# Optimization experiments

Measured on AMD Instinct MI355X. Metric: run time of the kernel, lower is better.

## Reference

```python
import jax, jax.numpy as jnp
import numpy as np

BN_EPS = 1e-5
HIDDEN = 64
NUM_LAYERS = 8


def setup_inputs() -> dict:
    key = jax.random.key(0)
    ks = jax.random.split(key, 24)
    N, E, G = 100000, 1600000, 500
    H, L = HIDDEN, NUM_LAYERS
    rn = lambda k, s, sc=0.1: jax.random.normal(k, s, jnp.float32) * sc
    un = lambda k, s: jax.random.uniform(k, s, jnp.float32, 0.5, 1.5)
    inp = {}
    inp["x"] = jax.random.normal(ks[0], (N, 1), jnp.float32)
    inp["edge_index"] = jax.random.randint(ks[1], (2, E), 0, N, jnp.int32)
    inp["batch"] = jnp.sort(jax.random.randint(ks[2], (N,), 0, G, jnp.int32))
    inp["num_graphs"] = G
    inp["eps"] = rn(ks[3], (L,))
    inp["W1_first"] = rn(ks[4], (1, H))
    inp["W1_rest"] = rn(ks[5], (L - 1, H, H))
    inp["b1"] = rn(ks[6], (L, H))
    inp["g1"] = un(ks[7], (L, H))
    inp["be1"] = rn(ks[8], (L, H))
    inp["m1"] = rn(ks[9], (L, H))
    inp["v1"] = un(ks[10], (L, H))
    inp["W2"] = rn(ks[11], (L, H, H))
    inp["b2"] = rn(ks[12], (L, H))
    inp["g2"] = un(ks[13], (L, H))
    inp["be2"] = rn(ks[14], (L, H))
    inp["m2"] = rn(ks[15], (L, H))
    inp["v2"] = un(ks[16], (L, H))
    inp["lin1_w"] = rn(ks[17], (L * H, H), 0.05)
    inp["lin1_b"] = rn(ks[18], (H,))
    inp["lin2_w"] = rn(ks[19], (H, 3))
    inp["lin2_b"] = rn(ks[20], (3,))
    return inp


def _bn(h, g, b, m, v):
    # BatchNorm1d in eval mode: affine normalize with running stats
    return (h - m) * jax.lax.rsqrt(v + BN_EPS) * g + b


def reference(x, edge_index, batch, num_graphs, eps, W1_first, W1_rest, b1, g1,
              be1, m1, v1, W2, b2, g2, be2, m2, v2, lin1_w, lin1_b, lin2_w, lin2_b):
    src, dst = edge_index[0], edge_index[1]
    N = x.shape[0]
    h = x
    xs = []
    for i in range(NUM_LAYERS):
        # GINConv: scatter-add neighbor aggregation + (1+eps)*self, then MLP
        agg = jax.ops.segment_sum(h[src], dst, num_segments=N)  # [N, H_in]
        z = (1.0 + eps[i]) * h + agg
        W1 = W1_first if i == 0 else W1_rest[i - 1]
        z = jnp.maximum(z @ W1 + b1[i], 0.0)
        z = _bn(z, g1[i], be1[i], m1[i], v1[i])
        z = jnp.maximum(z @ W2[i] + b2[i], 0.0)
        z = _bn(z, g2[i], be2[i], m2[i], v2[i])
        h = z
        xs.append(h)
    jk = jnp.concatenate(xs, axis=-1)  # [N, L*H] JumpingKnowledge 'cat'
    sums = jax.ops.segment_sum(jk, batch, num_segments=num_graphs)
    counts = jax.ops.segment_sum(jnp.ones((N,), jk.dtype), batch, num_segments=num_graphs)
    pooled = sums / jnp.maximum(counts, 1.0)[:, None]  # global_mean_pool
    h = jnp.maximum(pooled @ lin1_w + lin1_b, 0.0)
    # dropout is identity in eval mode
    logits = h @ lin2_w + lin2_b
    return jax.nn.log_softmax(logits, axis=-1)
```

## Files before the change

kernel.cpp:

```cpp
#include <hip/hip_runtime.h>
#include <hip/hip_bf16.h>
#include <math.h>


typedef unsigned int uint;
typedef unsigned short ushort;
typedef __attribute__((ext_vector_type(8))) short short8;
typedef __attribute__((ext_vector_type(4))) float floatx4;
typedef __attribute__((ext_vector_type(4))) uint uintx4;

#define BBITS 10
#define BCAP 20480
#define BMASK ((1 << BBITS) - 1)

__device__ __forceinline__ float bf_lo(uint w) { return __uint_as_float(w << 16); }
__device__ __forceinline__ float bf_hi(uint w) { return __uint_as_float(w & 0xffff0000u); }

__device__ __forceinline__ ushort f2bf(float x) {
  __hip_bfloat16 h = __float2bfloat16(x);
  return *(ushort*)&h;
}
__device__ __forceinline__ float bf2f(ushort u) { return __uint_as_float((uint)u << 16); }

__device__ __forceinline__ uint pack_bf16(float a, float b) {
  return (uint)f2bf(a) | ((uint)f2bf(b) << 16);
}

__device__ __forceinline__ void split8(float4 u0, float4 u1, short8& hi, short8& lo) {
  float v0 = u0.x, v1 = u0.y, v2 = u0.z, v3 = u0.w;
  float v4 = u1.x, v5 = u1.y, v6 = u1.z, v7 = u1.w;
  ushort h0 = f2bf(v0), h1 = f2bf(v1), h2 = f2bf(v2), h3 = f2bf(v3);
  ushort h4 = f2bf(v4), h5 = f2bf(v5), h6 = f2bf(v6), h7 = f2bf(v7);
  hi[0] = (short)h0; hi[1] = (short)h1; hi[2] = (short)h2; hi[3] = (short)h3;
  hi[4] = (short)h4; hi[5] = (short)h5; hi[6] = (short)h6; hi[7] = (short)h7;
  lo[0] = (short)f2bf(v0 - bf2f(h0)); lo[1] = (short)f2bf(v1 - bf2f(h1));
  lo[2] = (short)f2bf(v2 - bf2f(h2)); lo[3] = (short)f2bf(v3 - bf2f(h3));
  lo[4] = (short)f2bf(v4 - bf2f(h4)); lo[5] = (short)f2bf(v5 - bf2f(h5));
  lo[6] = (short)f2bf(v6 - bf2f(h6)); lo[7] = (short)f2bf(v7 - bf2f(h7));
}


__global__ void init_bc_kernel(int* __restrict__ bc, int NB) {
  int b = threadIdx.x;
  if (b < NB) bc[b * 16] = b * BCAP;
}

__global__ __launch_bounds__(1024) void bin_edges_kernel(
    const int* __restrict__ src, const int* __restrict__ dst, int* __restrict__ bc,
    uint* __restrict__ arena, int E) {
  __shared__ int cnt[128], base[128];
  for (long chunk = (long)blockIdx.x * 4096; chunk < E; chunk += (long)gridDim.x * 4096) {
    if (threadIdx.x < 128) cnt[threadIdx.x] = 0;
    __syncthreads();
    uint v[4];
    int b[4], r[4];
#pragma unroll
    for (int u = 0; u < 4; ++u) {
      long e = chunk + threadIdx.x + u * 1024;
      if (e < E) {
        int s = src[e];
        int d = dst[e];
        b[u] = d >> BBITS;
        v[u] = ((uint)s << BBITS) | (uint)(d & BMASK);
        r[u] = atomicAdd(&cnt[b[u]], 1);
      }
    }
    __syncthreads();
    if (threadIdx.x < 128)
      base[threadIdx.x] = cnt[threadIdx.x] ? atomicAdd(&bc[threadIdx.x * 16], cnt[threadIdx.x]) : 0;
    __syncthreads();
#pragma unroll
    for (int u = 0; u < 4; ++u) {
      long e = chunk + threadIdx.x + u * 1024;
      if (e < E) arena[base[b[u]] + r[u]] = v[u];
    }
    __syncthreads();
  }
}

__global__ __launch_bounds__(1024) void bucket_count_kernel(
    const uint* __restrict__ arena, const int* __restrict__ bc,
    int* __restrict__ deg, int N) {
  __shared__ int hist[1 << BBITS];
  int b = blockIdx.x;
  int lo = b << BBITS;
  int hi = min(lo + (1 << BBITS), N);
  hist[threadIdx.x] = 0;
  __syncthreads();
  int cnt = bc[b * 16] - b * BCAP;
  const uint* ad = arena + (size_t)b * BCAP;
  for (int i = threadIdx.x; i < cnt; i += 1024) atomicAdd(&hist[ad[i] & BMASK], 1);
  __syncthreads();
  if (lo + (int)threadIdx.x < hi) deg[lo + threadIdx.x] = hist[threadIdx.x];
}

__global__ __launch_bounds__(1024) void bucket_scatter_kernel(
    const uint* __restrict__ arena, const int* __restrict__ bc,
    const int* __restrict__ rp, int* __restrict__ col, int N) {
  __shared__ int cur[1 << BBITS];
  int b = blockIdx.x;
  int lo = b << BBITS;
  int hi = min(lo + (1 << BBITS), N);
  if (lo + (int)threadIdx.x < hi) cur[threadIdx.x] = rp[lo + threadIdx.x];
  __syncthreads();
  int cnt = bc[b * 16] - b * BCAP;
  const uint* ad = arena + (size_t)b * BCAP;
  for (int i = threadIdx.x; i < cnt; i += 1024) {
    uint v = ad[i];
    int pos = atomicAdd(&cur[v & BMASK], 1);
    col[pos] = (int)(v >> BBITS);
  }
}

__global__ void scan_blocksums(const int* __restrict__ deg, int* __restrict__ bsum, int N) {
  __shared__ int red[256];
  int i = blockIdx.x * 256 + threadIdx.x;
  red[threadIdx.x] = (i < N) ? deg[i] : 0;
  __syncthreads();
  for (int off = 128; off > 0; off >>= 1) {
    if (threadIdx.x < off) red[threadIdx.x] += red[threadIdx.x + off];
    __syncthreads();
  }
  if (threadIdx.x == 0) bsum[blockIdx.x] = red[0];
}

__global__ void scan_bsum(const int* __restrict__ bsum, int* __restrict__ boff,
                          int* __restrict__ rp_last, int B) {
  __shared__ int tmp[1024];
  int t = threadIdx.x;
  int v = (t < B) ? bsum[t] : 0;
  tmp[t] = v;
  __syncthreads();
  for (int off = 1; off < 1024; off <<= 1) {
    int u = (t >= off) ? tmp[t - off] : 0;
    __syncthreads();
    tmp[t] += u;
    __syncthreads();
  }
  if (t < B) boff[t] = tmp[t] - v;
  if (t == 1023) *rp_last = tmp[1023];
}

__global__ void scan_final(const int* __restrict__ deg, const int* __restrict__ boff,
                           int* __restrict__ rp, int N) {
  __shared__ int tmp[256];
  int i = blockIdx.x * 256 + threadIdx.x;
  int v = (i < N) ? deg[i] : 0;
  tmp[threadIdx.x] = v;
  __syncthreads();
  for (int off = 1; off < 256; off <<= 1) {
    int u = (threadIdx.x >= off) ? tmp[threadIdx.x - off] : 0;
    __syncthreads();
    tmp[threadIdx.x] += u;
    __syncthreads();
  }
  if (i < N) rp[i] = boff[blockIdx.x] + tmp[threadIdx.x] - v;
}

__global__ void graph_bounds_kernel(const int* __restrict__ batch, int* __restrict__ gs,
                                    int N, int G) {
  int n = blockIdx.x * 256 + threadIdx.x;
  if (n >= N) return;
  int b = batch[n];
  int bp = (n == 0) ? -1 : batch[n - 1];
  for (int g = bp + 1; g <= b; ++g) gs[g] = n;
  if (n == N - 1)
    for (int g = b + 1; g <= G; ++g) gs[g] = N;
}

__global__ void prepack_w_kernel(const float* __restrict__ W1_rest,
                                 const float* __restrict__ W2, ushort* __restrict__ wp) {
  int l = blockIdx.x >> 1, g = blockIdx.x & 1;
  const float* W;
  if (g == 0) {
    if (l == 0) return;
    W = W1_rest + (size_t)(l - 1) * 4096;
  } else {
    W = W2 + (size_t)l * 4096;
  }
  ushort* out = wp + (size_t)(l * 2 + g) * 8192;
  for (int idx = threadIdx.x; idx < 4096; idx += blockDim.x) {
    int j = idx & 7, lane = (idx >> 3) & 63, ks = (idx >> 9) & 1, nt = (idx >> 10) & 3;
    int k = ks * 32 + (lane >> 4) * 8 + j;
    int n = nt * 16 + (lane & 15);
    float w = W[k * 64 + n];
    ushort hi = f2bf(w);
    ushort lo = f2bf(w - bf2f(hi));
    size_t base = (size_t)((nt * 2 + ks) * 2) * 512 + lane * 8 + j;
    out[base] = hi;
    out[base + 512] = lo;
  }
}

__global__ __launch_bounds__(256, 8) void agg_kernel(
    const ushort* __restrict__ hb, const int* __restrict__ rp,
    const int* __restrict__ col, const float* __restrict__ eps,
    int layer, ushort* __restrict__ zb, int N) {
  int lane = threadIdx.x & 63;
  int g = lane >> 3;
  int r = lane & 7;
  int wave = blockIdx.x * (blockDim.x >> 6) + (threadIdx.x >> 6);
  int nwaves = gridDim.x * (blockDim.x >> 6);
  float ep = 1.0f + eps[layer];
  for (int n = wave * 2; n < N; n += nwaves * 2) {
    int n0 = __builtin_amdgcn_readfirstlane(n);
    int n1 = n0 + 1;
    int beg0 = rp[n0];
    int end0 = rp[n0 + 1];
    int end1 = (n1 < N) ? rp[n1 + 1] : end0;
    float a0[8] = {0.f, 0.f, 0.f, 0.f, 0.f, 0.f, 0.f, 0.f};
    float a1[8] = {0.f, 0.f, 0.f, 0.f, 0.f, 0.f, 0.f, 0.f};
    float b0[8] = {0.f, 0.f, 0.f, 0.f, 0.f, 0.f, 0.f, 0.f};
    float b1v[8] = {0.f, 0.f, 0.f, 0.f, 0.f, 0.f, 0.f, 0.f};
    int e0 = beg0 + g;
    int e1 = end0 + g;
    while (e0 < end0 || e1 < end1) {
      if (e0 < end0) {
        int s = col[e0];
        uint4 w = ((const uint4*)(hb + (long)s * 64))[r];
        a0[0] += bf_lo(w.x); a0[1] += bf_hi(w.x);
        a0[2] += bf_lo(w.y); a0[3] += bf_hi(w.y);
        a0[4] += bf_lo(w.z); a0[5] += bf_hi(w.z);
        a0[6] += bf_lo(w.w); a0[7] += bf_hi(w.w);
      }
      if (e0 + 8 < end0) {
        int s = col[e0 + 8];
        uint4 w = ((const uint4*)(hb + (long)s * 64))[r];
        a1[0] += bf_lo(w.x); a1[1] += bf_hi(w.x);
        a1[2] += bf_lo(w.y); a1[3] += bf_hi(w.y);
        a1[4] += bf_lo(w.z); a1[5] += bf_hi(w.z);
        a1[6] += bf_lo(w.w); a1[7] += bf_hi(w.w);
      }
      if (e1 < end1) {
        int s = col[e1];
        uint4 w = ((const uint4*)(hb + (long)s * 64))[r];
        b0[0] += bf_lo(w.x); b0[1] += bf_hi(w.x);
        b0[2] += bf_lo(w.y); b0[3] += bf_hi(w.y);
        b0[4] += bf_lo(w.z); b0[5] += bf_hi(w.z);
        b0[6] += bf_lo(w.w); b0[7] += bf_hi(w.w);
      }
      if (e1 + 8 < end1) {
        int s = col[e1 + 8];
        uint4 w = ((const uint4*)(hb + (long)s * 64))[r];
        b1v[0] += bf_lo(w.x); b1v[1] += bf_hi(w.x);
        b1v[2] += bf_lo(w.y); b1v[3] += bf_hi(w.y);
        b1v[4] += bf_lo(w.z); b1v[5] += bf_hi(w.z);
        b1v[6] += bf_lo(w.w); b1v[7] += bf_hi(w.w);
      }
      e0 += 16; e1 += 16;
    }
#pragma unroll
    for (int j = 0; j < 8; ++j) { a0[j] += a1[j]; b0[j] += b1v[j]; }
#pragma unroll
    for (int m = 8; m <= 32; m <<= 1) {
#pragma unroll
      for (int j = 0; j < 8; ++j) {
        a0[j] += __shfl_xor(a0[j], m, 64);
        b0[j] += __shfl_xor(b0[j], m, 64);
      }
    }
    if (g == 0) {
      uint4 hv = ((const uint4*)(hb + (long)n0 * 64))[r];
      float v0 = fmaf(ep, bf_lo(hv.x), a0[0]), v1 = fmaf(ep, bf_hi(hv.x), a0[1]);
      float v2 = fmaf(ep, bf_lo(hv.y), a0[2]), v3 = fmaf(ep, bf_hi(hv.y), a0[3]);
      float v4 = fmaf(ep, bf_lo(hv.z), a0[4]), v5 = fmaf(ep, bf_hi(hv.z), a0[5]);
      float v6 = fmaf(ep, bf_lo(hv.w), a0[6]), v7 = fmaf(ep, bf_hi(hv.w), a0[7]);
      uintx4 w;
      w.x = pack_bf16(v0, v1); w.y = pack_bf16(v2, v3);
      w.z = pack_bf16(v4, v5); w.w = pack_bf16(v6, v7);
      __builtin_nontemporal_store(w, (uintx4*)(zb + (size_t)n0 * 64 + r * 8));
    } else if (g == 1 && n1 < N) {
      uint4 hv = ((const uint4*)(hb + (long)n1 * 64))[r];
      float v0 = fmaf(ep, bf_lo(hv.x), b0[0]), v1 = fmaf(ep, bf_hi(hv.x), b0[1]);
      float v2 = fmaf(ep, bf_lo(hv.y), b0[2]), v3 = fmaf(ep, bf_hi(hv.y), b0[3]);
      float v4 = fmaf(ep, bf_lo(hv.z), b0[4]), v5 = fmaf(ep, bf_hi(hv.z), b0[5]);
      float v6 = fmaf(ep, bf_lo(hv.w), b0[6]), v7 = fmaf(ep, bf_hi(hv.w), b0[7]);
      uintx4 w;
      w.x = pack_bf16(v0, v1); w.y = pack_bf16(v2, v3);
      w.z = pack_bf16(v4, v5); w.w = pack_bf16(v6, v7);
      __builtin_nontemporal_store(w, (uintx4*)(zb + (size_t)n1 * 64 + r * 8));
    }
  }
}

__global__ __launch_bounds__(512) void mfma_mlp_kernel(
    const ushort* __restrict__ zb, const float* __restrict__ z0,
    const float* __restrict__ W1f, ushort* __restrict__ hout,
    const ushort* __restrict__ wp1, const ushort* __restrict__ wp2,
    const float* __restrict__ b1, const float* __restrict__ g1,
    const float* __restrict__ be1, const float* __restrict__ m1,
    const float* __restrict__ v1,
    const float* __restrict__ b2, const float* __restrict__ g2,
    const float* __restrict__ be2, const float* __restrict__ m2,
    const float* __restrict__ v2,
    const int* __restrict__ batch, float* __restrict__ pooled,
    int layer, int skip1, int N) {
  __shared__ float bnp[6][64];
  __shared__ float w1fl[64];
  __shared__ float sbuf[128][68];
  __shared__ int batchl[128];
  int tid = threadIdx.x;
  int blockbase = blockIdx.x * 128;
  if (tid < 64) {
    bnp[0][tid] = b1[tid];
    float s1 = g1[tid] * rsqrtf(v1[tid] + 1e-5f);
    bnp[1][tid] = s1;
    bnp[2][tid] = be1[tid] - m1[tid] * s1;
    bnp[3][tid] = b2[tid];
    float s2 = g2[tid] * rsqrtf(v2[tid] + 1e-5f);
    bnp[4][tid] = s2;
    bnp[5][tid] = be2[tid] - m2[tid] * s2;
    if (skip1) w1fl[tid] = W1f[tid];
  }
  if (tid < 128) batchl[tid] = (blockbase + tid < N) ? batch[blockbase + tid] : -1;
  __syncthreads();
  int wave = tid >> 6, lane = tid & 63;
  int q = lane >> 4, c = lane & 15;
  int base = blockbase + wave * 16;
  int srow = wave * 16;

  short8 ahi0, alo0, ahi1, alo1;
  if (!skip1) {
    {
      long row = base + c;
      if (row >= N) row = N - 1;
      const ushort* zr = zb + row * 64;
      ahi0 = __builtin_nontemporal_load((const short8*)(zr + q * 8));
      ahi1 = __builtin_nontemporal_load((const short8*)(zr + 32 + q * 8));
    }
    floatx4 acc[4];
#pragma unroll
    for (int nt = 0; nt < 4; ++nt) acc[nt] = (floatx4){0.f, 0.f, 0.f, 0.f};
#pragma unroll
    for (int nt = 0; nt < 4; ++nt) {
#pragma unroll
      for (int ks = 0; ks < 2; ++ks) {
        const ushort* fb = wp1 + ((nt * 2 + ks) * 2) * 512 + lane * 8;
        short8 bh = *(const short8*)fb;
        short8 bl = *(const short8*)(fb + 512);
        short8 ah = ks ? ahi1 : ahi0;
        acc[nt] = __builtin_amdgcn_mfma_f32_16x16x32_bf16(ah, bh, acc[nt], 0, 0, 0);
        acc[nt] = __builtin_amdgcn_mfma_f32_16x16x32_bf16(ah, bl, acc[nt], 0, 0, 0);
      }
    }
#pragma unroll
    for (int nt = 0; nt < 4; ++nt) {
      int feat = nt * 16 + c;
      float s1 = bnp[1][feat], o1 = bnp[2][feat], bb = bnp[0][feat];
#pragma unroll
      for (int r = 0; r < 4; ++r) {
        float y = fmaxf(acc[nt][r] + bb, 0.f);
        sbuf[srow + q * 4 + r][feat] = fmaf(y, s1, o1);
      }
    }
    float4 u0 = *(const float4*)&sbuf[srow + c][q * 8];
    float4 u1 = *(const float4*)&sbuf[srow + c][q * 8 + 4];
    split8(u0, u1, ahi0, alo0);
    u0 = *(const float4*)&sbuf[srow + c][32 + q * 8];
    u1 = *(const float4*)&sbuf[srow + c][32 + q * 8 + 4];
    split8(u0, u1, ahi1, alo1);
  } else {
    long row = base + c;
    if (row >= N) row = N - 1;
    float zv = z0[row];
    float4 t00, t01, t10, t11;
    {
      float tv[8];
#pragma unroll
      for (int j = 0; j < 8; ++j) {
        int k = q * 8 + j;
        float y = fmaxf(fmaf(zv, w1fl[k], bnp[0][k]), 0.f);
        tv[j] = fmaf(y, bnp[1][k], bnp[2][k]);
      }
      t00 = make_float4(tv[0], tv[1], tv[2], tv[3]);
      t01 = make_float4(tv[4], tv[5], tv[6], tv[7]);
#pragma unroll
      for (int j = 0; j < 8; ++j) {
        int k = 32 + q * 8 + j;
        float y = fmaxf(fmaf(zv, w1fl[k], bnp[0][k]), 0.f);
        tv[j] = fmaf(y, bnp[1][k], bnp[2][k]);
      }
      t10 = make_float4(tv[0], tv[1], tv[2], tv[3]);
      t11 = make_float4(tv[4], tv[5], tv[6], tv[7]);
    }
    split8(t00, t01, ahi0, alo0);
    split8(t10, t11, ahi1, alo1);
  }

  floatx4 acc2[4];
#pragma unroll
  for (int nt = 0; nt < 4; ++nt) acc2[nt] = (floatx4){0.f, 0.f, 0.f, 0.f};
#pragma unroll
  for (int nt = 0; nt < 4; ++nt) {
#pragma unroll
    for (int ks = 0; ks < 2; ++ks) {
      const ushort* fb = wp2 + ((nt * 2 + ks) * 2) * 512 + lane * 8;
      short8 bh = *(const short8*)fb;
      short8 bl = *(const short8*)(fb + 512);
      short8 ah = ks ? ahi1 : ahi0;
      short8 al = ks ? alo1 : alo0;
      acc2[nt] = __builtin_amdgcn_mfma_f32_16x16x32_bf16(ah, bh, acc2[nt], 0, 0, 0);
      acc2[nt] = __builtin_amdgcn_mfma_f32_16x16x32_bf16(al, bh, acc2[nt], 0, 0, 0);
      acc2[nt] = __builtin_amdgcn_mfma_f32_16x16x32_bf16(ah, bl, acc2[nt], 0, 0, 0);
    }
  }

#pragma unroll
  for (int nt = 0; nt < 4; ++nt) {
    int feat = nt * 16 + c;
    float s2 = bnp[4][feat], o2 = bnp[5][feat], bb = bnp[3][feat];
#pragma unroll
    for (int r = 0; r < 4; ++r) {
      int node = base + q * 4 + r;
      float val = 0.f;
      if (node < N) {
        float y = fmaxf(acc2[nt][r] + bb, 0.f);
        val = fmaf(y, s2, o2);
      }
      sbuf[srow + q * 4 + r][feat] = val;
    }
  }
  __syncthreads();

#pragma unroll
  for (int it = 0; it < 2; ++it) {
    int chunk = tid + it * 512;
    int row = chunk >> 3, c8 = chunk & 7;
    int node = blockbase + row;
    if (node < N) {
      const float* sp = &sbuf[row][c8 * 8];
      uintx4 w;
      w.x = pack_bf16(sp[0], sp[1]);
      w.y = pack_bf16(sp[2], sp[3]);
      w.z = pack_bf16(sp[4], sp[5]);
      w.w = pack_bf16(sp[6], sp[7]);
      *(uintx4*)(hout + (long)node * 64 + c8 * 8) = w;
    }
  }

  if (tid < 256) {
    int j = tid & 63;
    int quarter = tid >> 6;
    int nvalid = N - blockbase;
    if (nvalid > 128) nvalid = 128;
    int i = quarter * 32;
    int iend = i + 32;
    if (iend > nvalid) iend = nvalid;
    while (i < iend) {
      int g = batchl[i];
      float s = 0.f;
      while (i < iend && batchl[i] == g) { s += sbuf[i][j]; ++i; }
      atomicAdd(&pooled[(size_t)g * 512 + layer * 64 + j], s);
    }
  }
}

__global__ void z0_kernel(const float* __restrict__ x, const int* __restrict__ rp,
                          const int* __restrict__ col, const float* __restrict__ eps,
                          float* __restrict__ z0, int N) {
  int n = blockIdx.x * blockDim.x + threadIdx.x;
  if (n >= N) return;
  int beg = rp[n], end = rp[n + 1];
  float a = 0.f;
  for (int e = beg; e < end; ++e) a += x[col[e]];
  z0[n] = fmaf(1.0f + eps[0], x[n], a);
}

__global__ __launch_bounds__(64) void final_kernel(
    const float* __restrict__ pooled, const int* __restrict__ gs,
    const float* __restrict__ lin1_w, const float* __restrict__ lin1_b,
    const float* __restrict__ lin2_w, const float* __restrict__ lin2_b,
    float* __restrict__ out, int G) {
  int g = blockIdx.x;
  int j = threadIdx.x;
  float inv = 1.0f / fmaxf((float)(gs[g + 1] - gs[g]), 1.0f);
  __shared__ float p[512];
  for (int t = j; t < 512; t += 64) p[t] = pooled[(long)g * 512 + t] * inv;
  __syncthreads();
  float a0 = lin1_b[j], a1 = 0.f, a2 = 0.f, a3 = 0.f;
  for (int k = 0; k < 512; k += 4) {
    a0 = fmaf(p[k + 0], lin1_w[(k + 0) * 64 + j], a0);
    a1 = fmaf(p[k + 1], lin1_w[(k + 1) * 64 + j], a1);
    a2 = fmaf(p[k + 2], lin1_w[(k + 2) * 64 + j], a2);
    a3 = fmaf(p[k + 3], lin1_w[(k + 3) * 64 + j], a3);
  }
  float hv = fmaxf((a0 + a1) + (a2 + a3), 0.f);
  __shared__ float hb[64];
  hb[j] = hv;
  __syncthreads();
  __shared__ float lg[3];
  if (j < 3) {
    float a = lin2_b[j];
#pragma unroll
    for (int k = 0; k < 64; ++k) a = fmaf(hb[k], lin2_w[k * 3 + j], a);
    lg[j] = a;
  }
  __syncthreads();
  if (j < 3) {
    float mx = fmaxf(fmaxf(lg[0], lg[1]), lg[2]);
    float lse = mx + logf(expf(lg[0] - mx) + expf(lg[1] - mx) + expf(lg[2] - mx));
    out[g * 3 + j] = lg[j] - lse;
  }
}

extern "C" void kernel_launch(void* const* d_in, const int* in_sizes, int n_in,
                              void* d_out, int out_size, void* d_ws, size_t ws_size,
                              hipStream_t stream) {
  const float* x        = (const float*)d_in[0];
  const int*   edge     = (const int*)d_in[1];
  const int*   batch    = (const int*)d_in[2];
  const float* eps      = (const float*)d_in[4];
  const float* W1_first = (const float*)d_in[5];
  const float* W1_rest  = (const float*)d_in[6];
  const float* b1       = (const float*)d_in[7];
  const float* g1       = (const float*)d_in[8];
  const float* be1      = (const float*)d_in[9];
  const float* m1       = (const float*)d_in[10];
  const float* v1       = (const float*)d_in[11];
  const float* W2       = (const float*)d_in[12];
  const float* b2       = (const float*)d_in[13];
  const float* g2       = (const float*)d_in[14];
  const float* be2      = (const float*)d_in[15];
  const float* m2       = (const float*)d_in[16];
  const float* v2       = (const float*)d_in[17];
  const float* lin1_w   = (const float*)d_in[18];
  const float* lin1_b   = (const float*)d_in[19];
  const float* lin2_w   = (const float*)d_in[20];
  const float* lin2_b   = (const float*)d_in[21];

  int N = in_sizes[0];
  int E = in_sizes[1] / 2;
  int G = out_size / 3;
  const int* esrc = edge;
  const int* edst = edge + E;
  int NB = (N + (1 << BBITS) - 1) >> BBITS;
  if (NB > 128) NB = 128;

  size_t off = 0;
  auto alloc = [&](size_t bytes) -> char* {
    char* p = (char*)d_ws + off;
    off += (bytes + 255) & ~(size_t)255;
    return p;
  };
  int SB = (N + 255) / 256;
  int*    deg    = (int*)alloc((size_t)N * 4);
  int*    rp     = (int*)alloc((size_t)(N + 1) * 4);
  int*    col    = (int*)alloc((size_t)E * 4);
  int*    bsum   = (int*)alloc((size_t)SB * 4);
  int*    boff   = (int*)alloc((size_t)SB * 4);
  int*    bc     = (int*)alloc((size_t)128 * 16 * 4);
  uint*   arena  = (uint*)alloc((size_t)NB * BCAP * 4);
  int*    gs     = (int*)alloc((size_t)(G + 1) * 4);
  ushort* wpack  = (ushort*)alloc((size_t)16 * 8192 * 2);
  float*  z0buf  = (float*)alloc((size_t)N * 4);
  ushort* zbuf   = (ushort*)alloc((size_t)N * 64 * 2);
  ushort* hA     = (ushort*)alloc((size_t)N * 64 * 2);
  ushort* hB     = (ushort*)alloc((size_t)N * 64 * 2);
  float*  pooled = (float*)alloc((size_t)G * 512 * 4);
  (void)ws_size;

  init_bc_kernel<<<1, 128, 0, stream>>>(bc, NB);
  int ebA = (E + 4095) / 4096;
  bin_edges_kernel<<<ebA, 1024, 0, stream>>>(esrc, edst, bc, arena, E);
  bucket_count_kernel<<<NB, 1024, 0, stream>>>(arena, bc, deg, N);
  scan_blocksums<<<SB, 256, 0, stream>>>(deg, bsum, N);
  scan_bsum<<<1, 1024, 0, stream>>>(bsum, boff, rp + N, SB);
  scan_final<<<SB, 256, 0, stream>>>(deg, boff, rp, N);
  bucket_scatter_kernel<<<NB, 1024, 0, stream>>>(arena, bc, rp, col, N);

  graph_bounds_kernel<<<SB, 256, 0, stream>>>(batch, gs, N, G);
  prepack_w_kernel<<<16, 256, 0, stream>>>(W1_rest, W2, wpack);
  (void)hipMemsetAsync(pooled, 0, (size_t)G * 512 * 4, stream);

  int nb = (N + 127) / 128;
  z0_kernel<<<SB, 256, 0, stream>>>(x, rp, col, eps, z0buf, N);
  mfma_mlp_kernel<<<nb, 512, 0, stream>>>(zbuf, z0buf, W1_first, hA,
      wpack, wpack + 8192,
      b1, g1, be1, m1, v1, b2, g2, be2, m2, v2, batch, pooled, 0, 1, N);

  ushort* hin = hA;
  ushort* hout = hB;
  for (int i = 1; i < 8; ++i) {
    agg_kernel<<<2048, 256, 0, stream>>>(hin, rp, col, eps, i, zbuf, N);
    mfma_mlp_kernel<<<nb, 512, 0, stream>>>(zbuf, z0buf, W1_first, hout,
        wpack + (size_t)(2 * i) * 8192, wpack + (size_t)(2 * i + 1) * 8192,
        b1 + i * 64, g1 + i * 64, be1 + i * 64, m1 + i * 64, v1 + i * 64,
        b2 + i * 64, g2 + i * 64, be2 + i * 64, m2 + i * 64, v2 + i * 64,
        batch, pooled, i, 0, N);
    ushort* t = hin; hin = hout; hout = t;
  }
  final_kernel<<<G, 64, 0, stream>>>(pooled, gs, lin1_w, lin1_b,
                                     lin2_w, lin2_b, (float*)d_out, G);
}
```

Measured before the change: 632.6 us.

## Remap aggregation waves to four nodes with two edge slots each

The CSR gather kernel now processes four nodes per wave, with 16 lanes per node split into two edge slots, instead of two nodes with eight slots each. Each slot issues four independent row loads per iteration, using clamped indices and 0/1 mask multipliers instead of branches, and the col reads become nontemporal loads. This is meant to raise lane use on low-degree nodes (average degree is about 16), reduce divergence and cut the three-level shuffle reduction to one step. In exchange, masked slots issue redundant loads, and nodes of very different degree within a wave serialise the loop.

```diff
diff --git a/kernel.cpp b/kernel.cpp
--- a/kernel.cpp
+++ b/kernel.cpp
@@ -24,6 +24,10 @@
 
 __device__ __forceinline__ uint pack_bf16(float a, float b) {
   return (uint)f2bf(a) | ((uint)f2bf(b) << 16);
+}
+
+__device__ __forceinline__ float slot_combine(float v) {
+  return v + __shfl_xor(v, 8, 64);
 }
 
 __device__ __forceinline__ void split8(float4 u0, float4 u1, short8& hi, short8& lo) {
@@ -197,88 +201,65 @@
     const int* __restrict__ col, const float* __restrict__ eps,
     int layer, ushort* __restrict__ zb, int N) {
   int lane = threadIdx.x & 63;
-  int g = lane >> 3;
+  int ni = lane >> 4;
+  int s = (lane >> 3) & 1;
   int r = lane & 7;
   int wave = blockIdx.x * (blockDim.x >> 6) + (threadIdx.x >> 6);
   int nwaves = gridDim.x * (blockDim.x >> 6);
   float ep = 1.0f + eps[layer];
-  for (int n = wave * 2; n < N; n += nwaves * 2) {
-    int n0 = __builtin_amdgcn_readfirstlane(n);
-    int n1 = n0 + 1;
-    int beg0 = rp[n0];
-    int end0 = rp[n0 + 1];
-    int end1 = (n1 < N) ? rp[n1 + 1] : end0;
-    float a0[8] = {0.f, 0.f, 0.f, 0.f, 0.f, 0.f, 0.f, 0.f};
-    float a1[8] = {0.f, 0.f, 0.f, 0.f, 0.f, 0.f, 0.f, 0.f};
-    float b0[8] = {0.f, 0.f, 0.f, 0.f, 0.f, 0.f, 0.f, 0.f};
-    float b1v[8] = {0.f, 0.f, 0.f, 0.f, 0.f, 0.f, 0.f, 0.f};
-    int e0 = beg0 + g;
-    int e1 = end0 + g;
-    while (e0 < end0 || e1 < end1) {
-      if (e0 < end0) {
-        int s = col[e0];
-        uint4 w = ((const uint4*)(hb + (long)s * 64))[r];
-        a0[0] += bf_lo(w.x); a0[1] += bf_hi(w.x);
-        a0[2] += bf_lo(w.y); a0[3] += bf_hi(w.y);
-        a0[4] += bf_lo(w.z); a0[5] += bf_hi(w.z);
-        a0[6] += bf_lo(w.w); a0[7] += bf_hi(w.w);
-      }
-      if (e0 + 8 < end0) {
-        int s = col[e0 + 8];
-        uint4 w = ((const uint4*)(hb + (long)s * 64))[r];
-        a1[0] += bf_lo(w.x); a1[1] += bf_hi(w.x);
-        a1[2] += bf_lo(w.y); a1[3] += bf_hi(w.y);
-        a1[4] += bf_lo(w.z); a1[5] += bf_hi(w.z);
-        a1[6] += bf_lo(w.w); a1[7] += bf_hi(w.w);
-      }
-      if (e1 < end1) {
-        int s = col[e1];
-        uint4 w = ((const uint4*)(hb + (long)s * 64))[r];
-        b0[0] += bf_lo(w.x); b0[1] += bf_hi(w.x);
-        b0[2] += bf_lo(w.y); b0[3] += bf_hi(w.y);
-        b0[4] += bf_lo(w.z); b0[5] += bf_hi(w.z);
-        b0[6] += bf_lo(w.w); b0[7] += bf_hi(w.w);
-      }
-      if (e1 + 8 < end1) {
-        int s = col[e1 + 8];
-        uint4 w = ((const uint4*)(hb + (long)s * 64))[r];
-        b1v[0] += bf_lo(w.x); b1v[1] += bf_hi(w.x);
-        b1v[2] += bf_lo(w.y); b1v[3] += bf_hi(w.y);
-        b1v[4] += bf_lo(w.z); b1v[5] += bf_hi(w.z);
-        b1v[6] += bf_lo(w.w); b1v[7] += bf_hi(w.w);
-      }
-      e0 += 16; e1 += 16;
-    }
-#pragma unroll
-    for (int j = 0; j < 8; ++j) { a0[j] += a1[j]; b0[j] += b1v[j]; }
-#pragma unroll
-    for (int m = 8; m <= 32; m <<= 1) {
-#pragma unroll
-      for (int j = 0; j < 8; ++j) {
-        a0[j] += __shfl_xor(a0[j], m, 64);
-        b0[j] += __shfl_xor(b0[j], m, 64);
-      }
-    }
-    if (g == 0) {
-      uint4 hv = ((const uint4*)(hb + (long)n0 * 64))[r];
-      float v0 = fmaf(ep, bf_lo(hv.x), a0[0]), v1 = fmaf(ep, bf_hi(hv.x), a0[1]);
-      float v2 = fmaf(ep, bf_lo(hv.y), a0[2]), v3 = fmaf(ep, bf_hi(hv.y), a0[3]);
-      float v4 = fmaf(ep, bf_lo(hv.z), a0[4]), v5 = fmaf(ep, bf_hi(hv.z), a0[5]);
-      float v6 = fmaf(ep, bf_lo(hv.w), a0[6]), v7 = fmaf(ep, bf_hi(hv.w), a0[7]);
+  for (int qb = wave * 4; qb < N; qb += nwaves * 4) {
+    int node = qb + ni;
+    bool valid = node < N;
+    int nn = valid ? node : (N - 1);
+    int beg = rp[nn];
+    int end = valid ? rp[nn + 1] : beg;
+    float a[8] = {0.f, 0.f, 0.f, 0.f, 0.f, 0.f, 0.f, 0.f};
+    int e = beg + s;
+    while (e < end) {
+      int e1 = (e + 2 < end) ? (e + 2) : e;
+      int e2 = (e + 4 < end) ? (e + 4) : e;
+      int e3 = (e + 6 < end) ? (e + 6) : e;
+      float m1 = (e + 2 < end) ? 1.0f : 0.0f;
+      float m2 = (e + 4 < end) ? 1.0f : 0.0f;
+      float m3 = (e + 6 < end) ? 1.0f : 0.0f;
+      int c0 = __builtin_nontemporal_load(col + e);
+      int c1 = __builtin_nontemporal_load(col + e1);
+      int c2 = __builtin_nontemporal_load(col + e2);
+      int c3 = __builtin_nontemporal_load(col + e3);
+      uint4 w0 = ((const uint4*)(hb + (long)c0 * 64))[r];
+      uint4 w1 = ((const uint4*)(hb + (long)c1 * 64))[r];
+      uint4 w2 = ((const uint4*)(hb + (long)c2 * 64))[r];
+      uint4 w3 = ((const uint4*)(hb + (long)c3 * 64))[r];
+      a[0] += bf_lo(w0.x); a[1] += bf_hi(w0.x);
+      a[2] += bf_lo(w0.y); a[3] += bf_hi(w0.y);
+      a[4] += bf_lo(w0.z); a[5] += bf_hi(w0.z);
+      a[6] += bf_lo(w0.w); a[7] += bf_hi(w0.w);
+      a[0] = fmaf(m1, bf_lo(w1.x), a[0]); a[1] = fmaf(m1, bf_hi(w1.x), a[1]);
+      a[2] = fmaf(m1, bf_lo(w1.y), a[2]); a[3] = fmaf(m1, bf_hi(w1.y), a[3]);
+      a[4] = fmaf(m1, bf_lo(w1.z), a[4]); a[5] = fmaf(m1, bf_hi(w1.z), a[5]);
+      a[6] = fmaf(m1, bf_lo(w1.w), a[6]); a[7] = fmaf(m1, bf_hi(w1.w), a[7]);
+      a[0] = fmaf(m2, bf_lo(w2.x), a[0]); a[1] = fmaf(m2, bf_hi(w2.x), a[1]);
+      a[2] = fmaf(m2, bf_lo(w2.y), a[2]); a[3] = fmaf(m2, bf_hi(w2.y), a[3]);
+      a[4] = fmaf(m2, bf_lo(w2.z), a[4]); a[5] = fmaf(m2, bf_hi(w2.z), a[5]);
+      a[6] = fmaf(m2, bf_lo(w2.w), a[6]); a[7] = fmaf(m2, bf_hi(w2.w), a[7]);
+      a[0] = fmaf(m3, bf_lo(w3.x), a[0]); a[1] = fmaf(m3, bf_hi(w3.x), a[1]);
+      a[2] = fmaf(m3, bf_lo(w3.y), a[2]); a[3] = fmaf(m3, bf_hi(w3.y), a[3]);
+      a[4] = fmaf(m3, bf_lo(w3.z), a[4]); a[5] = fmaf(m3, bf_hi(w3.z), a[5]);
+      a[6] = fmaf(m3, bf_lo(w3.w), a[6]); a[7] = fmaf(m3, bf_hi(w3.w), a[7]);
+      e += 8;
+    }
+#pragma unroll
+    for (int j = 0; j < 8; ++j) a[j] = slot_combine(a[j]);
+    if (s == 0 && valid) {
+      uint4 hv = ((const uint4*)(hb + (long)node * 64))[r];
+      float v0 = fmaf(ep, bf_lo(hv.x), a[0]), v1 = fmaf(ep, bf_hi(hv.x), a[1]);
+      float v2 = fmaf(ep, bf_lo(hv.y), a[2]), v3 = fmaf(ep, bf_hi(hv.y), a[3]);
+      float v4 = fmaf(ep, bf_lo(hv.z), a[4]), v5 = fmaf(ep, bf_hi(hv.z), a[5]);
+      float v6 = fmaf(ep, bf_lo(hv.w), a[6]), v7 = fmaf(ep, bf_hi(hv.w), a[7]);
       uintx4 w;
       w.x = pack_bf16(v0, v1); w.y = pack_bf16(v2, v3);
       w.z = pack_bf16(v4, v5); w.w = pack_bf16(v6, v7);
-      __builtin_nontemporal_store(w, (uintx4*)(zb + (size_t)n0 * 64 + r * 8));
-    } else if (g == 1 && n1 < N) {
-      uint4 hv = ((const uint4*)(hb + (long)n1 * 64))[r];
-      float v0 = fmaf(ep, bf_lo(hv.x), b0[0]), v1 = fmaf(ep, bf_hi(hv.x), b0[1]);
-      float v2 = fmaf(ep, bf_lo(hv.y), b0[2]), v3 = fmaf(ep, bf_hi(hv.y), b0[3]);
-      float v4 = fmaf(ep, bf_lo(hv.z), b0[4]), v5 = fmaf(ep, bf_hi(hv.z), b0[5]);
-      float v6 = fmaf(ep, bf_lo(hv.w), b0[6]), v7 = fmaf(ep, bf_hi(hv.w), b0[7]);
-      uintx4 w;
-      w.x = pack_bf16(v0, v1); w.y = pack_bf16(v2, v3);
-      w.z = pack_bf16(v4, v5); w.w = pack_bf16(v6, v7);
-      __builtin_nontemporal_store(w, (uintx4*)(zb + (size_t)n1 * 64 + r * 8));
+      __builtin_nontemporal_store(w, (uintx4*)(zb + (size_t)node * 64 + r * 8));
     }
   }
 }
```

Measured after the change: 573.0 us. -9.4%, faster.
